# Performance work log

Measured on AMD Instinct MI355X. Metric: run time of the kernel, lower is better.

## Reference

```python
import jax, jax.numpy as jnp
import numpy as np

G = 64        # number of graphs
N = 2048      # nodes per graph
D = 16        # fixed degree (neighbor list length per node)
N_ITER = 5    # WL iterations
NTOT = G * N
L = N + N_ITER * NTOT  # upper bound on total label ids (zero-padding doesn't change K)


def setup_inputs() -> dict:
    key = jax.random.key(0)
    k1, = jax.random.split(key, 1)
    # each node's neighbors live in the same graph: local idx + graph offset
    local = jax.random.randint(k1, (NTOT, D), 0, N, dtype=jnp.int32)
    offsets = ((jnp.arange(NTOT, dtype=jnp.int32) // N) * N)
    neighbors = local + offsets[:, None]
    # default label str(node) with a dict shared across graphs -> id = local node index
    init_labels = (jnp.arange(NTOT, dtype=jnp.int32) % N)
    node_weights = jnp.ones((NTOT,), jnp.float32)  # unit count per node (faithful)
    return {"neighbors": neighbors, "init_labels": init_labels,
            "node_weights": node_weights}


def _relabel(sig, offset):
    """Global WL relabel: identical signature rows -> same fresh id (>= offset).

    sig: [NTOT, D+1] int32, row = (own_label, sorted neighbor labels).
    Id assignment order differs from first-occurrence order but that is a pure
    permutation of ids within the iteration and leaves K = F F^T unchanged.
    """
    perm = jnp.lexsort(sig.T)                      # group identical rows together
    s = sig[perm]
    is_new = jnp.concatenate(
        [jnp.ones((1,), bool), jnp.any(s[1:] != s[:-1], axis=1)])
    rank = jnp.cumsum(is_new.astype(jnp.int32)) - 1
    new_labels = jnp.zeros(sig.shape[0], sig.dtype).at[perm].set(
        offset + rank)
    return new_labels, offset + rank[-1] + 1


def _histogram(labels, graph_id, weights):
    """Per-graph label histogram -> [G, L] (scatter-add of node weights)."""
    flat = graph_id * L + labels                   # max ~42M, fits int32
    return jnp.zeros(G * L, weights.dtype).at[flat].add(weights).reshape(G, L)


def reference(neighbors, init_labels, node_weights):
    graph_id = jnp.arange(NTOT, dtype=jnp.int32) // N
    labels = init_labels
    F = _histogram(labels, graph_id, node_weights)
    offset = jnp.asarray(N, jnp.int32)             # label_counter after init
    for _ in range(N_ITER):
        nbr_labels = jnp.sort(labels[neighbors], axis=1)   # [NTOT, D]
        sig = jnp.concatenate([labels[:, None], nbr_labels], axis=1)
        labels, offset = _relabel(sig, offset)
        F = F + _histogram(labels, graph_id, node_weights)
    K = F @ F.T                                     # [G, G]
    diag = jnp.sqrt(jnp.diag(K))
    return K / (diag[None, :] * diag[:, None])
```

## Files before the change

kernel.cpp:

```cpp
#include <hip/hip_runtime.h>

constexpr int G_ = 64;
constexpr int N_ = 2048;
constexpr int D_ = 16;
constexpr int N_ITER_ = 5;
constexpr int NTOT_ = G_ * N_;
constexpr int TS_ = 1 << 18;
constexpr unsigned TMASK_ = TS_ - 1;

using u64 = unsigned long long;

__device__ __forceinline__ int ald(const int* p) {
    return __hip_atomic_load(p, __ATOMIC_RELAXED, __HIP_MEMORY_SCOPE_AGENT);
}
__device__ __forceinline__ u64 ald64(const u64* p) {
    return __hip_atomic_load(p, __ATOMIC_RELAXED, __HIP_MEMORY_SCOPE_AGENT);
}
__device__ __forceinline__ float aldf(const float* p) {
    return __hip_atomic_load(p, __ATOMIC_RELAXED, __HIP_MEMORY_SCOPE_AGENT);
}
__device__ __forceinline__ void ast(int* p, int v) {
    __hip_atomic_store(p, v, __ATOMIC_RELAXED, __HIP_MEMORY_SCOPE_AGENT);
}

__device__ __forceinline__ int lidx(int u) { return ((u & (N_ - 1)) << 6) | (u >> 11); }

__device__ __forceinline__ u64 fmix64(u64 h) {
    h ^= h >> 33; h *= 0xff51afd7ed558ccdULL;
    h ^= h >> 33; h *= 0xc4ceb9fe1a85ec53ULL;
    h ^= h >> 33; return h;
}
__device__ __forceinline__ unsigned fmix32(unsigned h) {
    h ^= h >> 16; h *= 0x85ebca6bu;
    h ^= h >> 13; h *= 0xc2b2ae35u;
    h ^= h >> 16; return h;
}

__device__ __forceinline__ void sort16(int v[16]) {
    #pragma unroll
    for (int k = 2; k <= 16; k <<= 1) {
        #pragma unroll
        for (int j = k >> 1; j > 0; j >>= 1) {
            #pragma unroll
            for (int i = 0; i < 16; ++i) {
                int l = i ^ j;
                if (l > i) {
                    int a = v[i], b = v[l];
                    bool up = ((i & k) == 0);
                    if (up ? (a > b) : (a < b)) { v[i] = b; v[l] = a; }
                }
            }
        }
    }
}

__device__ __forceinline__ void gather16(const int* __restrict__ nbrs,
                                         const int* lold, int node, int v[16]) {
    const int4* np = reinterpret_cast<const int4*>(nbrs + (size_t)node * D_);
    int4 n0 = np[0], n1 = np[1], n2 = np[2], n3 = np[3];
    int idx[16] = {n0.x, n0.y, n0.z, n0.w, n1.x, n1.y, n1.z, n1.w,
                   n2.x, n2.y, n2.z, n2.w, n3.x, n3.y, n3.z, n3.w};
    #pragma unroll
    for (int i = 0; i < 16; ++i) v[i] = ald(&lold[lidx(idx[i])]);
}

__device__ __forceinline__ int wl_insert_one(int u, int t,
                                             const int* __restrict__ nbrs,
                                             const int* lold,
                                             u64* tab, int* head, int* next_) {
    const int own = ald(&lold[lidx(u)]);
    int v[16];
    gather16(nbrs, lold, u, v);
    sort16(v);
    u64 h = 1469598103934665603ULL;
    h = (h ^ (unsigned)own) * 1099511628211ULL;
    #pragma unroll
    for (int k = 0; k < 16; ++k) h = (h ^ (unsigned)v[k]) * 1099511628211ULL;
    h = fmix64(h);

    const u64 HM = ~((1ULL << 21) - 1);
    const u64 itg = (u64)(t + 1) << 18;
    const u64 mine = (h & HM) | itg | (u64)(u + 1);
    unsigned slot = (unsigned)h & TMASK_;
    int rep = -1;
    u64 seen = ald64(&tab[slot]);
    while (true) {
        if (((seen >> 18) & 7) == (u64)(t + 1)) {
            bool matched = false;
            if ((seen & HM) == (h & HM)) {
                const int r = (int)(seen & 0x3FFFFULL) - 1;
                if (ald(&lold[lidx(r)]) == own) {
                    int w2[16];
                    gather16(nbrs, lold, r, w2);
                    sort16(w2);
                    bool eq = true;
                    #pragma unroll
                    for (int k = 0; k < 16; ++k) eq &= (w2[k] == v[k]);
                    if (eq) { rep = r; matched = true; }
                }
            }
            if (matched) break;
            slot = (slot + 1) & TMASK_;
            seen = ald64(&tab[slot]);
        } else {
            u64 old = atomicCAS(&tab[slot], seen, mine);
            if (old == seen) { rep = u; break; }
            seen = old;
        }
    }
    next_[u] = atomicExch(&head[rep], (int)(((unsigned)(t + 1) << 18) | (unsigned)(u + 1)));
    return rep;
}

__device__ __forceinline__ void wl_outer_multi(u64 mm, int hd, unsigned itertag1,
                                               const float* __restrict__ wts,
                                               const int* next_, float* K, int lane) {
    while (mm) {
        const int src = __ffsll((long long)mm) - 1; mm &= mm - 1;
        int m = __shfl(hd, src, 64);
        float v = 0.f;
        while ((((unsigned)m) >> 18) == itertag1) {
            const int node = (m & 0x3FFFF) - 1;
            const float wm = wts[node];
            if (lane == (node >> 11)) v += wm;
            m = ald(&next_[node]);
        }
        #pragma unroll 8
        for (int h0 = 1; h0 < 64; ++h0) {
            const int hh = (h0 + lane) & 63;
            const float vh = __shfl(v, hh, 64);
            const float p = v * vh;
            if (p != 0.f) atomicAdd(&K[lane * 64 + hh], p);
        }
    }
}

__global__ __launch_bounds__(256) void wl_main_k(const int* __restrict__ nbrs,
                                                 const float* __restrict__ wts,
                                                 int* __restrict__ labA,
                                                 int* __restrict__ labB,
                                                 u64* __restrict__ actmask,
                                                 float* __restrict__ K) {
    const int tid = threadIdx.x;
    if (blockIdx.x >= 512) {
        const int g = blockIdx.x - 512;
        const float4* w4 = reinterpret_cast<const float4*>(wts);
        __shared__ float4 rowg[N_ / 4];
        for (int i = tid; i < N_ / 4; i += 256) rowg[i] = w4[(size_t)g * (N_ / 4) + i];
        __syncthreads();
        const int h = tid & 63, chunk = tid >> 6;
        float acc = 0.f;
        for (int i = 0; i < 128; ++i) {
            float4 a = rowg[chunk * 128 + i];
            float4 b = w4[(size_t)h * (N_ / 4) + chunk * 128 + i];
            acc += a.x * b.x + a.y * b.y + a.z * b.z + a.w * b.w;
        }
        __shared__ float part[256];
        part[tid] = acc;
        __syncthreads();
        if (tid < 64) {
            float s = part[tid] + part[tid + 64] + part[tid + 128] + part[tid + 192];
            K[g * 64 + tid] = (tid == g) ? 6.f * s : s;
        }
        return;
    }
    const int lane = tid & 63;
    const int l = (blockIdx.x * 256 + tid) >> 6;
    const int u = lane * N_ + l;
    const int4* np = reinterpret_cast<const int4*>(nbrs + (size_t)u * D_);
    int4 n0 = np[0], n1 = np[1], n2 = np[2], n3 = np[3];
    int raw[16] = {n0.x, n0.y, n0.z, n0.w, n1.x, n1.y, n1.z, n1.w,
                   n2.x, n2.y, n2.z, n2.w, n3.x, n3.y, n3.z, n3.w};
    int v[16];
    unsigned h = 0;
    #pragma unroll
    for (int i = 0; i < 16; ++i) {
        v[i] = raw[i] & (N_ - 1);
        h += fmix32((unsigned)(v[i] + 1));
    }
    u64 mask = 0;
    #pragma unroll
    for (int j = 0; j < 64; ++j) {
        unsigned hj = __shfl(h, j, 64);
        mask |= (u64)(hj == h) << j;
    }
    const u64 self = 1ULL << lane;
    if (__ballot(mask != self)) {
        sort16(v);
        u64 em = 0;
        for (int j = 0; j < 64; ++j) {
            bool eq = true;
            #pragma unroll
            for (int k = 0; k < 16; ++k) eq &= (__shfl(v[k], j, 64) == v[k]);
            em |= (u64)eq << j;
        }
        mask = em;
    }
    const int rep = (__ffsll((long long)mask) - 1) * N_ + l;
    const int li = (l << 6) | lane;
    labA[li] = rep;
    labB[li] = rep;
    const u64 act = __ballot(mask != self);
    if (lane == 0) actmask[l] = act;
}

__global__ __launch_bounds__(256) void wl_tail_k(const int* __restrict__ nbrs,
                                                 const float* __restrict__ wts,
                                                 int* __restrict__ labA,
                                                 int* __restrict__ labB,
                                                 u64* __restrict__ tab,
                                                 int* __restrict__ head,
                                                 int* __restrict__ next_,
                                                 int* __restrict__ listA,
                                                 int* __restrict__ listB,
                                                 const u64* __restrict__ actmask,
                                                 float* __restrict__ K,
                                                 float* __restrict__ out) {
    const int tid = threadIdx.x;
    const int lane = tid & 63;
    __shared__ int scnt[2];
    if (tid < 2) scnt[tid] = 0;
    __syncthreads();
    for (int w = tid; w < N_; w += 256) {
        u64 m = ald64(&actmask[w]);
        while (m) {
            const int g = __ffsll((long long)m) - 1; m &= m - 1;
            const int pos = atomicAdd(&scnt[0], 1);
            listA[pos] = g * N_ + w;
        }
    }
    __syncthreads();
    const int nA0 = scnt[0];

    if (nA0 > 0) {
        for (int i = 0; i < nA0; ++i) {
            const int u = ald(&listA[i]);
            const int ru = ald(&labA[lidx(u)]);
            const float wu = wts[u];
            for (int j = tid; j < nA0; j += 256) {
                if (j == i) continue;
                const int vnode = ald(&listA[j]);
                if (ald(&labA[lidx(vnode)]) == ru)
                    atomicAdd(&K[(u >> 11) * 64 + (vnode >> 11)], wu * wts[vnode]);
            }
        }
        for (int i = tid; i < TS_; i += 256) tab[i] = 0ULL;
        for (int i = tid; i < NTOT_; i += 256) head[i] = 0;
        __syncthreads();

        for (int t = 1; t < N_ITER_; ++t) {
            const int odd = t & 1;
            int* lold_ = odd ? labA : labB;
            int* lnew_ = odd ? labB : labA;
            int* slist = odd ? listA : listB;
            int* dlist = odd ? listB : listA;
            const int sIdx = odd ^ 1, dIdx = odd;
            if (tid == 0) scnt[dIdx] = 0;
            __syncthreads();
            const int nA = scnt[sIdx];
            const unsigned tg = (unsigned)(t + 1) << 18;
            for (int i = tid; i < nA; i += 256) {
                const int u = ald(&slist[i]);
                const int rep = wl_insert_one(u, t, nbrs, lold_, tab, head, next_);
                ast(&lnew_[lidx(u)], rep);
            }
            __syncthreads();
            const int rounds = (nA + 255) >> 8;
            for (int r0 = 0; r0 < rounds; ++r0) {
                const int i = r0 * 256 + tid;
                const bool has = i < nA;
                int u = 0, hd = 0, nx = 0;
                bool owner = false, single = false;
                if (has) {
                    u = ald(&slist[i]);
                    const int rep = ald(&lnew_[lidx(u)]);
                    owner = (rep == u);
                    if (owner) { hd = ald(&head[u]); nx = ald(&next_[u]); }
                    single = owner && ((unsigned)hd == (tg | (unsigned)(u + 1)))
                                   && (((unsigned)nx >> 18) != (unsigned)(t + 1));
                    if (single) {
                        ast(&labA[lidx(u)], u);
                        ast(&labB[lidx(u)], u);
                    } else {
                        const int pos = atomicAdd(&scnt[dIdx], 1);
                        ast(&dlist[pos], u);
                    }
                }
                wl_outer_multi(__ballot(owner && !single), hd, (unsigned)(t + 1),
                               wts, next_, K, lane);
            }
            __syncthreads();
        }
    }
    for (int i = tid; i < G_ * G_; i += 256) {
        const int g = i >> 6, h = i & 63;
        const float kgh = aldf(&K[i]);
        const float kgg = aldf(&K[g * 64 + g]);
        const float khh = aldf(&K[h * 64 + h]);
        out[i] = kgh * rsqrtf(kgg * khh);
    }
}

extern "C" void kernel_launch(void* const* d_in, const int* in_sizes, int n_in,
                              void* d_out, int out_size, void* d_ws, size_t ws_size,
                              hipStream_t stream) {
    const int* nbrs = (const int*)d_in[0];
    const float* wts = (const float*)d_in[2];
    float* out = (float*)d_out;

    char* ws = (char*)d_ws;
    size_t off = 0;
    auto alloc = [&](size_t bytes) { void* p = ws + off; off += (bytes + 255) & ~(size_t)255; return p; };
    u64* tab = (u64*)alloc((size_t)TS_ * 8);
    int* head = (int*)alloc((size_t)NTOT_ * 4);
    int* next_ = (int*)alloc((size_t)NTOT_ * 4);
    int* labA = (int*)alloc((size_t)NTOT_ * 4);
    int* labB = (int*)alloc((size_t)NTOT_ * 4);
    int* listA = (int*)alloc((size_t)NTOT_ * 4);
    int* listB = (int*)alloc((size_t)NTOT_ * 4);
    u64* actmask = (u64*)alloc((size_t)N_ * 8);
    float* K = (float*)alloc((size_t)G_ * G_ * 4);
    if (off > ws_size) return;

    wl_main_k<<<576, 256, 0, stream>>>(nbrs, wts, labA, labB, actmask, K);
    wl_tail_k<<<1, 256, 0, stream>>>(nbrs, wts, labA, labB, tab, head, next_,
                                     listA, listB, actmask, K, out);
}
```

Measured before the change: 30.85 us.

## Fuse main and tail kernels via grid-wide completion counter

Result: slower. 41.31 us (+33.9%).

```diff
diff --git a/kernel.cpp b/kernel.cpp
--- a/kernel.cpp
+++ b/kernel.cpp
@@ -7,6 +7,7 @@
 constexpr int NTOT_ = G_ * N_;
 constexpr int TS_ = 1 << 18;
 constexpr unsigned TMASK_ = TS_ - 1;
+constexpr int NBLK_ = 576;
 
 using u64 = unsigned long long;
 
@@ -20,6 +21,12 @@
     return __hip_atomic_load(p, __ATOMIC_RELAXED, __HIP_MEMORY_SCOPE_AGENT);
 }
 __device__ __forceinline__ void ast(int* p, int v) {
+    __hip_atomic_store(p, v, __ATOMIC_RELAXED, __HIP_MEMORY_SCOPE_AGENT);
+}
+__device__ __forceinline__ void ast64(u64* p, u64 v) {
+    __hip_atomic_store(p, v, __ATOMIC_RELAXED, __HIP_MEMORY_SCOPE_AGENT);
+}
+__device__ __forceinline__ void astf(float* p, float v) {
     __hip_atomic_store(p, v, __ATOMIC_RELAXED, __HIP_MEMORY_SCOPE_AGENT);
 }
 
@@ -135,17 +142,28 @@
     }
 }
 
-__global__ __launch_bounds__(256) void wl_main_k(const int* __restrict__ nbrs,
-                                                 const float* __restrict__ wts,
-                                                 int* __restrict__ labA,
-                                                 int* __restrict__ labB,
-                                                 u64* __restrict__ actmask,
-                                                 float* __restrict__ K) {
+__global__ __launch_bounds__(256, 4) void wl_all_k(const int* __restrict__ nbrs,
+                                                   const float* __restrict__ wts,
+                                                   int* __restrict__ labA,
+                                                   int* __restrict__ labB,
+                                                   u64* __restrict__ tab,
+                                                   int* __restrict__ head,
+                                                   int* __restrict__ next_,
+                                                   int* __restrict__ listA,
+                                                   int* __restrict__ listB,
+                                                   u64* __restrict__ actmask,
+                                                   float* __restrict__ K,
+                                                   u64* __restrict__ done,
+                                                   float* __restrict__ out) {
     const int tid = threadIdx.x;
+    const int lane = tid & 63;
+    __shared__ float4 rowg[N_ / 4];
+    __shared__ float part[256];
+    __shared__ int scnt[2];
+
     if (blockIdx.x >= 512) {
         const int g = blockIdx.x - 512;
         const float4* w4 = reinterpret_cast<const float4*>(wts);
-        __shared__ float4 rowg[N_ / 4];
         for (int i = tid; i < N_ / 4; i += 256) rowg[i] = w4[(size_t)g * (N_ / 4) + i];
         __syncthreads();
         const int h = tid & 63, chunk = tid >> 6;
@@ -155,70 +173,62 @@
             float4 b = w4[(size_t)h * (N_ / 4) + chunk * 128 + i];
             acc += a.x * b.x + a.y * b.y + a.z * b.z + a.w * b.w;
         }
-        __shared__ float part[256];
         part[tid] = acc;
         __syncthreads();
         if (tid < 64) {
             float s = part[tid] + part[tid + 64] + part[tid + 128] + part[tid + 192];
-            K[g * 64 + tid] = (tid == g) ? 6.f * s : s;
-        }
-        return;
-    }
-    const int lane = tid & 63;
-    const int l = (blockIdx.x * 256 + tid) >> 6;
-    const int u = lane * N_ + l;
-    const int4* np = reinterpret_cast<const int4*>(nbrs + (size_t)u * D_);
-    int4 n0 = np[0], n1 = np[1], n2 = np[2], n3 = np[3];
-    int raw[16] = {n0.x, n0.y, n0.z, n0.w, n1.x, n1.y, n1.z, n1.w,
-                   n2.x, n2.y, n2.z, n2.w, n3.x, n3.y, n3.z, n3.w};
-    int v[16];
-    unsigned h = 0;
-    #pragma unroll
-    for (int i = 0; i < 16; ++i) {
-        v[i] = raw[i] & (N_ - 1);
-        h += fmix32((unsigned)(v[i] + 1));
-    }
-    u64 mask = 0;
-    #pragma unroll
-    for (int j = 0; j < 64; ++j) {
-        unsigned hj = __shfl(h, j, 64);
-        mask |= (u64)(hj == h) << j;
-    }
-    const u64 self = 1ULL << lane;
-    if (__ballot(mask != self)) {
-        sort16(v);
-        u64 em = 0;
+            astf(&K[g * 64 + tid], (tid == g) ? 6.f * s : s);
+        }
+    } else {
+        const int l = (blockIdx.x * 256 + tid) >> 6;
+        const int u = lane * N_ + l;
+        const int4* np = reinterpret_cast<const int4*>(nbrs + (size_t)u * D_);
+        int4 n0 = np[0], n1 = np[1], n2 = np[2], n3 = np[3];
+        int raw[16] = {n0.x, n0.y, n0.z, n0.w, n1.x, n1.y, n1.z, n1.w,
+                       n2.x, n2.y, n2.z, n2.w, n3.x, n3.y, n3.z, n3.w};
+        int v[16];
+        unsigned h = 0;
+        #pragma unroll
+        for (int i = 0; i < 16; ++i) {
+            v[i] = raw[i] & (N_ - 1);
+            h += fmix32((unsigned)(v[i] + 1));
+        }
+        u64 mask = 0;
+        #pragma unroll
         for (int j = 0; j < 64; ++j) {
-            bool eq = true;
-            #pragma unroll
-            for (int k = 0; k < 16; ++k) eq &= (__shfl(v[k], j, 64) == v[k]);
-            em |= (u64)eq << j;
-        }
-        mask = em;
-    }
-    const int rep = (__ffsll((long long)mask) - 1) * N_ + l;
-    const int li = (l << 6) | lane;
-    labA[li] = rep;
-    labB[li] = rep;
-    const u64 act = __ballot(mask != self);
-    if (lane == 0) actmask[l] = act;
-}
-
-__global__ __launch_bounds__(256) void wl_tail_k(const int* __restrict__ nbrs,
-                                                 const float* __restrict__ wts,
-                                                 int* __restrict__ labA,
-                                                 int* __restrict__ labB,
-                                                 u64* __restrict__ tab,
-                                                 int* __restrict__ head,
-                                                 int* __restrict__ next_,
-                                                 int* __restrict__ listA,
-                                                 int* __restrict__ listB,
-                                                 const u64* __restrict__ actmask,
-                                                 float* __restrict__ K,
-                                                 float* __restrict__ out) {
-    const int tid = threadIdx.x;
-    const int lane = tid & 63;
-    __shared__ int scnt[2];
+            unsigned hj = __shfl(h, j, 64);
+            mask |= (u64)(hj == h) << j;
+        }
+        const u64 self = 1ULL << lane;
+        if (__ballot(mask != self)) {
+            sort16(v);
+            u64 em = 0;
+            for (int j = 0; j < 64; ++j) {
+                bool eq = true;
+                #pragma unroll
+                for (int k = 0; k < 16; ++k) eq &= (__shfl(v[k], j, 64) == v[k]);
+                em |= (u64)eq << j;
+            }
+            mask = em;
+        }
+        const int rep = (__ffsll((long long)mask) - 1) * N_ + l;
+        const int li = (l << 6) | lane;
+        ast(&labA[li], rep);
+        ast(&labB[li], rep);
+        const u64 act = __ballot(mask != self);
+        if (lane == 0) ast64(&actmask[l], act);
+    }
+
+    __syncthreads();
+    if (tid == 0)
+        __hip_atomic_fetch_add(done, 1ULL, __ATOMIC_RELEASE, __HIP_MEMORY_SCOPE_AGENT);
+    if (blockIdx.x != 0) return;
+    if (tid == 0) {
+        while (__hip_atomic_load(done, __ATOMIC_ACQUIRE, __HIP_MEMORY_SCOPE_AGENT)
+               < (u64)NBLK_) { __builtin_amdgcn_s_sleep(1); }
+    }
+    __syncthreads();
+
     if (tid < 2) scnt[tid] = 0;
     __syncthreads();
     for (int w = tid; w < N_; w += 256) {
@@ -320,9 +330,10 @@
     int* listB = (int*)alloc((size_t)NTOT_ * 4);
     u64* actmask = (u64*)alloc((size_t)N_ * 8);
     float* K = (float*)alloc((size_t)G_ * G_ * 4);
+    u64* done = (u64*)alloc(256);
     if (off > ws_size) return;
 
-    wl_main_k<<<576, 256, 0, stream>>>(nbrs, wts, labA, labB, actmask, K);
-    wl_tail_k<<<1, 256, 0, stream>>>(nbrs, wts, labA, labB, tab, head, next_,
-                                     listA, listB, actmask, K, out);
-}
+    hipMemsetAsync(done, 0, 8, stream);
+    wl_all_k<<<NBLK_, 256, 0, stream>>>(nbrs, wts, labA, labB, tab, head, next_,
+                                        listA, listB, actmask, K, done, out);
+}
```
